# Performance work log

Measured on AMD Instinct MI355X. Metric: run time of the kernel, lower is better.

Reference implementation:

```python
import jax, jax.numpy as jnp
import numpy as np

N = 100000   # num nodes
E = 800000   # num edges
D = 16       # latent_dim
K = 3        # message-passing iterations
ALPHA = 0.1
GAMMA = 0.9


def _mlp2(x, w1, b1, w2, b2):
    return jax.nn.relu(x @ w1 + b1) @ w2 + b2


def setup_inputs() -> dict:
    key = jax.random.key(0)
    ks = iter(jax.random.split(key, 40))
    def w(shape, fan_in):
        return jax.random.normal(next(ks), shape, jnp.float32) / np.sqrt(fan_in)
    return {
        "edge_index": jax.random.randint(next(ks), (2, E), 0, N),
        "edge_attr": jax.random.normal(next(ks), (E, 3), jnp.float32),
        "a_ij": jax.random.normal(next(ks), (E, 1), jnp.float32),
        "prb_data": jax.random.normal(next(ks), (N, 1), jnp.float32),
        "sol": jax.random.normal(next(ks), (N, 1), jnp.float32),
        "y": jax.random.normal(next(ks), (N, 1), jnp.float32),
        "phi_to_w1": w((K, 2 * D + 3, D), 2 * D + 3), "phi_to_b1": jnp.zeros((K, D), jnp.float32),
        "phi_to_w2": w((K, D, D), D), "phi_to_b2": jnp.zeros((K, D), jnp.float32),
        "phi_from_w1": w((K, 2 * D + 3, D), 2 * D + 3), "phi_from_b1": jnp.zeros((K, D), jnp.float32),
        "phi_from_w2": w((K, D, D), D), "phi_from_b2": jnp.zeros((K, D), jnp.float32),
        "psi_w1": w((K, 3 * D + 1, D), 3 * D + 1), "psi_b1": jnp.zeros((K, D), jnp.float32),
        "psi_w2": w((K, D, D), D), "psi_b2": jnp.zeros((K, D), jnp.float32),
        "dec_w1": w((K, D, D), D), "dec_b1": jnp.zeros((K, D), jnp.float32),
        "dec_w2": w((K, D, 1), D), "dec_b2": jnp.zeros((K, 1), jnp.float32),
    }


def reference(edge_index, edge_attr, a_ij, prb_data, sol, y,
              phi_to_w1, phi_to_b1, phi_to_w2, phi_to_b2,
              phi_from_w1, phi_from_b1, phi_from_w2, phi_from_b2,
              psi_w1, psi_b1, psi_w2, psi_b2,
              dec_w1, dec_b1, dec_w2, dec_b2):
    src, dst = edge_index[0], edge_index[1]
    # remove_self_loops: with 'add' aggregation, zeroing self-loop messages is equivalent.
    sl_mask = (src != dst).astype(edge_attr.dtype)[:, None]

    def message_pass(h, xi_idx, xj_idx, agg_idx, w1, b1, w2, b2):
        # gather-concat-MLP-scatter: tmp is [E, 2D+3]
        tmp = jnp.concatenate([h[xi_idx], h[xj_idx], edge_attr], axis=1)
        m = _mlp2(tmp, w1, b1, w2, b2) * sl_mask
        return jax.ops.segment_sum(m, agg_idx, num_segments=N)

    a_val = a_ij[:, 0]
    def residual_loss(u):
        # SparseTensor(row=src, col=dst, value=a_ij) @ u  (self-loops kept here)
        Au = jax.ops.segment_sum(a_val * u[dst, 0], src, num_segments=N)[:, None]
        return jnp.mean((Au - y) ** 2)

    h = jnp.zeros((N, D), edge_attr.dtype)
    u = _mlp2(h, dec_w1[0], dec_b1[0], dec_w2[0], dec_b2[0])  # U['0']
    total_loss = jnp.zeros((), edge_attr.dtype)
    for t in range(K):
        # Phi_to: flow source_to_target -> x_i = h[dst], x_j = h[src], aggregate at dst
        mess_to = message_pass(h, dst, src, dst, phi_to_w1[t], phi_to_b1[t], phi_to_w2[t], phi_to_b2[t])
        # Phi_from: flow target_to_source -> x_i = h[src], x_j = h[dst], aggregate at src
        mess_from = message_pass(h, src, dst, src, phi_from_w1[t], phi_from_b1[t], phi_from_w2[t], phi_from_b2[t])
        concat = jnp.concatenate([h, mess_to, mess_from, prb_data], axis=1)  # [N, 3D+1]
        h = h + ALPHA * _mlp2(concat, psi_w1[t], psi_b1[t], psi_w2[t], psi_b2[t])
        u = _mlp2(h, dec_w1[t], dec_b1[t], dec_w2[t], dec_b2[t])
        total_loss = total_loss + residual_loss(u) * GAMMA ** (K - t - 1)
    return u, total_loss
```

## Files before the change

### kernel.cpp

```cpp
#include <hip/hip_runtime.h>

#define NN 100000
#define NE 800000
#define DD 16
#define ALPHA 0.1f

__device__ __forceinline__ void load16(const float* __restrict__ p, float* r) {
  float4 v0 = *(const float4*)(p + 0);
  float4 v1 = *(const float4*)(p + 4);
  float4 v2 = *(const float4*)(p + 8);
  float4 v3 = *(const float4*)(p + 12);
  r[0]=v0.x; r[1]=v0.y; r[2]=v0.z; r[3]=v0.w;
  r[4]=v1.x; r[5]=v1.y; r[6]=v1.z; r[7]=v1.w;
  r[8]=v2.x; r[9]=v2.y; r[10]=v2.z; r[11]=v2.w;
  r[12]=v3.x; r[13]=v3.y; r[14]=v3.z; r[15]=v3.w;
}

__device__ __forceinline__ void store16(float* __restrict__ p, const float* r) {
  *(float4*)(p + 0)  = make_float4(r[0], r[1], r[2], r[3]);
  *(float4*)(p + 4)  = make_float4(r[4], r[5], r[6], r[7]);
  *(float4*)(p + 8)  = make_float4(r[8], r[9], r[10], r[11]);
  *(float4*)(p + 12) = make_float4(r[12], r[13], r[14], r[15]);
}

__device__ __forceinline__ unsigned f2bf(float x) {
  unsigned b = __float_as_uint(x);
  return (b + 0x7FFFu + ((b >> 16) & 1u)) >> 16;
}

__global__ __launch_bounds__(256) void hist_kernel(
    const int* __restrict__ ei, int* __restrict__ hist,
    int* __restrict__ rank_dst, int* __restrict__ rank_src)
{
  int e = blockIdx.x * 256 + threadIdx.x;
  if (e >= NE) return;
  int s = ei[e];
  int d = ei[NE + e];
  rank_dst[e] = atomicAdd(&hist[d], 1);
  rank_src[e] = atomicAdd(&hist[NN + s], 1);
}

__global__ __launch_bounds__(256) void scan1_kernel(
    const int* __restrict__ in, int* __restrict__ out, int* __restrict__ sums, int L)
{
  __shared__ int sh[256];
  int t = threadIdx.x;
  int i0 = blockIdx.x * 1024 + t * 4;
  int v0 = (i0 + 0 < L) ? in[i0 + 0] : 0;
  int v1 = (i0 + 1 < L) ? in[i0 + 1] : 0;
  int v2 = (i0 + 2 < L) ? in[i0 + 2] : 0;
  int v3 = (i0 + 3 < L) ? in[i0 + 3] : 0;
  int tot = v0 + v1 + v2 + v3;
  sh[t] = tot;
  __syncthreads();
  int val = tot;
  for (int off = 1; off < 256; off <<= 1) {
    int x = (t >= off) ? sh[t - off] : 0;
    __syncthreads();
    val += x; sh[t] = val;
    __syncthreads();
  }
  if (t == 255) sums[blockIdx.x] = val;
  int run = val - tot;
  if (i0 + 0 < L) out[i0 + 0] = run; run += v0;
  if (i0 + 1 < L) out[i0 + 1] = run; run += v1;
  if (i0 + 2 < L) out[i0 + 2] = run; run += v2;
  if (i0 + 3 < L) out[i0 + 3] = run;
}

__global__ __launch_bounds__(256) void scan2_kernel(
    int* __restrict__ sums, int nb, int* __restrict__ out_total)
{
  __shared__ int sh[256];
  int t = threadIdx.x;
  int v = (t < nb) ? sums[t] : 0;
  sh[t] = v;
  __syncthreads();
  int val = v;
  for (int off = 1; off < 256; off <<= 1) {
    int x = (t >= off) ? sh[t - off] : 0;
    __syncthreads();
    val += x; sh[t] = val;
    __syncthreads();
  }
  if (t < nb) sums[t] = val - v;
  if (t == 255) *out_total = val;
}

__global__ __launch_bounds__(256) void scan3_kernel(
    int* __restrict__ out, const int* __restrict__ sums, int L)
{
  int i = blockIdx.x * 256 + threadIdx.x;
  if (i < L) out[i] += sums[i >> 10];
}

__global__ __launch_bounds__(256) void scatter_kernel(
    const int* __restrict__ ei, const float* __restrict__ ea, const float* __restrict__ a,
    const int* __restrict__ base,
    const int* __restrict__ rank_dst, const int* __restrict__ rank_src,
    float4* __restrict__ pay, float2* __restrict__ pay_au)
{
  int e = blockIdx.x * 256 + threadIdx.x;
  if (e >= NE) return;
  int s = ei[e];
  int d = ei[NE + e];
  float e0 = ea[3 * (size_t)e], e1 = ea[3 * (size_t)e + 1], e2 = ea[3 * (size_t)e + 2];
  int sl = (s == d);
  int pd = base[d] + rank_dst[e];
  pay[pd] = make_float4(__int_as_float(sl ? -1 : s), e0, e1, e2);
  int ps = base[NN + s] + rank_src[e];
  pay[ps] = make_float4(__int_as_float(sl ? -1 : d), e0, e1, e2);
  pay_au[ps - NE] = make_float2(__int_as_float(d), a[e]);
}

__global__ __launch_bounds__(256) void dbucket_kernel(
    const int* __restrict__ base, int* __restrict__ dhist)
{
  __shared__ int lh[64];
  int t = threadIdx.x;
  if (t < 64) lh[t] = 0;
  __syncthreads();
  int g = blockIdx.x * 256 + t;
  if (g < 2 * NN) {
    int dg = base[g + 1] - base[g];
    atomicAdd(&lh[min(dg, 63)], 1);
  }
  __syncthreads();
  if (t < 64 && lh[t]) atomicAdd(&dhist[t], lh[t]);
}

__global__ void dscan64_kernel(int* __restrict__ dhist)
{
  int t = threadIdx.x;
  int v = dhist[t];
  int x = v;
  #pragma unroll
  for (int off = 1; off < 64; off <<= 1) {
    int y = __shfl_up(x, off, 64);
    if (t >= off) x += y;
  }
  dhist[t] = x - v;
}

__global__ __launch_bounds__(256) void dperm_kernel(
    const int* __restrict__ base, int* __restrict__ dhist, int* __restrict__ perm)
{
  __shared__ int lh[64];
  __shared__ int lb[64];
  int t = threadIdx.x;
  if (t < 64) lh[t] = 0;
  __syncthreads();
  int g = blockIdx.x * 256 + t;
  int b = 0, r = 0;
  bool v = (g < 2 * NN);
  if (v) {
    int dg = base[g + 1] - base[g];
    b = min(dg, 63);
    r = atomicAdd(&lh[b], 1);
  }
  __syncthreads();
  if (t < 64 && lh[t]) lb[t] = atomicAdd(&dhist[t], lh[t]);
  __syncthreads();
  if (v) perm[lb[b] + r] = g;
}

template<bool FIRST, bool WITH_AU>
__global__ __launch_bounds__(256) void gather_kernel(
    const float* __restrict__ h, const unsigned short* __restrict__ hb,
    const float4* __restrict__ pay, const int* __restrict__ base,
    const int* __restrict__ perm,
    const float* __restrict__ to_w1, const float* __restrict__ to_b1,
    const float* __restrict__ to_w2, const float* __restrict__ to_b2,
    const float* __restrict__ fr_w1, const float* __restrict__ fr_b1,
    const float* __restrict__ fr_w2, const float* __restrict__ fr_b2,
    float* __restrict__ mto, float* __restrict__ mfr, int gblocks,
    const float2* __restrict__ pay_au, const float* __restrict__ u,
    const float* __restrict__ y, float w, float* __restrict__ loss)
{
  if (WITH_AU && (int)blockIdx.x >= gblocks) {
    __shared__ float ss[4];
    int n = (blockIdx.x - gblocks) * 256 + threadIdx.x;
    float acc = 0.0f;
    if (n < NN) {
      float au = 0.0f;
      int beg = base[NN + n] - NE, end = base[NN + n + 1] - NE;
      for (int i = beg; i < end; ++i) {
        float2 q = pay_au[i];
        au = fmaf(q.y, u[__float_as_int(q.x)], au);
      }
      float dlt = au - y[n];
      acc = dlt * dlt;
    }
    #pragma unroll
    for (int off = 32; off > 0; off >>= 1) acc += __shfl_down(acc, off);
    int lane = threadIdx.x & 63, wid = threadIdx.x >> 6;
    if (lane == 0) ss[wid] = acc;
    __syncthreads();
    if (threadIdx.x == 0) atomicAdd(loss, (ss[0] + ss[1] + ss[2] + ss[3]) * w);
    return;
  }

  __shared__ float sw[1696];
  __shared__ float p1buf[512];
  int t = threadIdx.x;
  for (int i = t; i < 560; i += 256) { sw[i] = to_w1[i]; sw[848 + i] = fr_w1[i]; }
  { int i = t;
    if (i < 256) { sw[576 + i] = to_w2[i]; sw[848 + 576 + i] = fr_w2[i]; }
    if (i < 16) {
      sw[560 + i] = to_b1[i];
      sw[832 + i] = to_b2[i];
      sw[848 + 560 + i] = fr_b1[i];
      sw[848 + 832 + i] = fr_b2[i];
    }
  }
  __syncthreads();

  int sub = (blockIdx.x * 256 + t) >> 3;
  int l = t & 7;
  int g = perm[sub];
  int dir = (g >= NN) ? 1 : 0;
  int n = g - (dir ? NN : 0);

  const float* w1 = sw + (dir ? 848 : 0);
  const float* b1 = w1 + 560;
  const float* w2 = w1 + 576;
  const float* b2 = w1 + 832;

  float p1v[DD];
  if (FIRST) {
    #pragma unroll
    for (int j = 0; j < DD; ++j) p1v[j] = b1[j];
  } else {
    float hv[DD];
    load16(h + (size_t)n * DD, hv);
    int j0 = 2 * l;
    float pa = b1[j0], pb = b1[j0 + 1];
    #pragma unroll
    for (int k = 0; k < DD; ++k) {
      pa = fmaf(hv[k], w1[k * DD + j0], pa);
      pb = fmaf(hv[k], w1[k * DD + j0 + 1], pb);
    }
    p1buf[2 * t] = pa;
    p1buf[2 * t + 1] = pb;
    __syncthreads();
    const float* pbase = &p1buf[(t & ~7) * 2];
    #pragma unroll
    for (int j = 0; j < DD; ++j) p1v[j] = pbase[j];
  }

  float hs_[DD];
  #pragma unroll
  for (int j = 0; j < DD; ++j) hs_[j] = 0.0f;
  int cnt = 0;

  int beg = base[g], end = base[g + 1];
  for (int i = beg + l; i < end; i += 8) {
    float4 q = pay[i];
    int nb = __float_as_int(q.x);
    if (nb >= 0) {
      float hid[DD];
      #pragma unroll
      for (int j = 0; j < DD; ++j)
        hid[j] = fmaf(q.y, w1[32 * DD + j],
                 fmaf(q.z, w1[33 * DD + j],
                 fmaf(q.w, w1[34 * DD + j], p1v[j])));
      if (!FIRST) {
        uint4 qa = *(const uint4*)(hb + (size_t)nb * DD);
        uint4 qb = *(const uint4*)(hb + (size_t)nb * DD + 8);
        float hv[DD];
        hv[0]  = __uint_as_float(qa.x << 16); hv[1]  = __uint_as_float(qa.x & 0xFFFF0000u);
        hv[2]  = __uint_as_float(qa.y << 16); hv[3]  = __uint_as_float(qa.y & 0xFFFF0000u);
        hv[4]  = __uint_as_float(qa.z << 16); hv[5]  = __uint_as_float(qa.z & 0xFFFF0000u);
        hv[6]  = __uint_as_float(qa.w << 16); hv[7]  = __uint_as_float(qa.w & 0xFFFF0000u);
        hv[8]  = __uint_as_float(qb.x << 16); hv[9]  = __uint_as_float(qb.x & 0xFFFF0000u);
        hv[10] = __uint_as_float(qb.y << 16); hv[11] = __uint_as_float(qb.y & 0xFFFF0000u);
        hv[12] = __uint_as_float(qb.z << 16); hv[13] = __uint_as_float(qb.z & 0xFFFF0000u);
        hv[14] = __uint_as_float(qb.w << 16); hv[15] = __uint_as_float(qb.w & 0xFFFF0000u);
        #pragma unroll
        for (int k = 0; k < DD; ++k) {
          float x = hv[k];
          #pragma unroll
          for (int j = 0; j < DD; ++j) hid[j] = fmaf(x, w1[(DD + k) * DD + j], hid[j]);
        }
      }
      #pragma unroll
      for (int j = 0; j < DD; ++j) hs_[j] += fmaxf(hid[j], 0.0f);
      ++cnt;
    }
  }

  #pragma unroll
  for (int j = 0; j < DD; ++j) {
    hs_[j] += __shfl_xor(hs_[j], 1, 64);
    hs_[j] += __shfl_xor(hs_[j], 2, 64);
    hs_[j] += __shfl_xor(hs_[j], 4, 64);
  }
  cnt += __shfl_xor(cnt, 1, 64);
  cnt += __shfl_xor(cnt, 2, 64);
  cnt += __shfl_xor(cnt, 4, 64);

  float c = (float)cnt;
  float m0 = c * b2[2 * l + 0];
  float m1 = c * b2[2 * l + 1];
  #pragma unroll
  for (int k = 0; k < DD; ++k) {
    float x = hs_[k];
    m0 = fmaf(x, w2[k * DD + 2 * l + 0], m0);
    m1 = fmaf(x, w2[k * DD + 2 * l + 1], m1);
  }
  float* dst = (dir ? mfr : mto) + (size_t)n * DD + 2 * l;
  *(float2*)dst = make_float2(m0, m1);
}

__global__ __launch_bounds__(256) void node_kernel(
    float* __restrict__ h, unsigned short* __restrict__ hb,
    const float* __restrict__ mto, const float* __restrict__ mfr,
    const float* __restrict__ prb,
    const float* __restrict__ psi_w1, const float* __restrict__ psi_b1,
    const float* __restrict__ psi_w2, const float* __restrict__ psi_b2,
    const float* __restrict__ dec_w1, const float* __restrict__ dec_b1,
    const float* __restrict__ dec_w2, const float* __restrict__ dec_b2,
    float* __restrict__ u)
{
  __shared__ float sw[1361];
  for (int i = threadIdx.x; i < 784; i += 256) sw[i] = psi_w1[i];
  { int i = threadIdx.x;
    if (i < 256) { sw[800 + i] = psi_w2[i]; sw[1072 + i] = dec_w1[i]; }
    if (i < 16) {
      sw[784 + i] = psi_b1[i];
      sw[1056 + i] = psi_b2[i];
      sw[1328 + i] = dec_b1[i];
      sw[1344 + i] = dec_w2[i];
    }
    if (i == 0) sw[1360] = dec_b2[0];
  }
  __syncthreads();

  int n = blockIdx.x * 256 + threadIdx.x;
  if (n >= NN) return;

  float hv[DD], mt[DD], mf[DD];
  load16(h + (size_t)n * DD, hv);
  load16(mto + (size_t)n * DD, mt);
  load16(mfr + (size_t)n * DD, mf);
  float p = prb[n];

  float hid[DD];
  #pragma unroll
  for (int j = 0; j < DD; ++j) hid[j] = sw[784 + j];
  #pragma unroll
  for (int i = 0; i < DD; ++i) {
    float x = hv[i];
    #pragma unroll
    for (int j = 0; j < DD; ++j) hid[j] = fmaf(x, sw[i * DD + j], hid[j]);
  }
  #pragma unroll
  for (int i = 0; i < DD; ++i) {
    float x = mt[i];
    #pragma unroll
    for (int j = 0; j < DD; ++j) hid[j] = fmaf(x, sw[(DD + i) * DD + j], hid[j]);
  }
  #pragma unroll
  for (int i = 0; i < DD; ++i) {
    float x = mf[i];
    #pragma unroll
    for (int j = 0; j < DD; ++j) hid[j] = fmaf(x, sw[(2 * DD + i) * DD + j], hid[j]);
  }
  #pragma unroll
  for (int j = 0; j < DD; ++j) hid[j] = fmaf(p, sw[48 * DD + j], hid[j]);
  #pragma unroll
  for (int j = 0; j < DD; ++j) hid[j] = fmaxf(hid[j], 0.0f);

  float hnew[DD];
  #pragma unroll
  for (int j = 0; j < DD; ++j) hnew[j] = sw[1056 + j];
  #pragma unroll
  for (int i = 0; i < DD; ++i) {
    float x = hid[i];
    #pragma unroll
    for (int j = 0; j < DD; ++j) hnew[j] = fmaf(x, sw[800 + i * DD + j], hnew[j]);
  }
  #pragma unroll
  for (int j = 0; j < DD; ++j) hnew[j] = fmaf(ALPHA, hnew[j], hv[j]);
  store16(h + (size_t)n * DD, hnew);

  uint4 pa, pb;
  pa.x = f2bf(hnew[0])  | (f2bf(hnew[1])  << 16);
  pa.y = f2bf(hnew[2])  | (f2bf(hnew[3])  << 16);
  pa.z = f2bf(hnew[4])  | (f2bf(hnew[5])  << 16);
  pa.w = f2bf(hnew[6])  | (f2bf(hnew[7])  << 16);
  pb.x = f2bf(hnew[8])  | (f2bf(hnew[9])  << 16);
  pb.y = f2bf(hnew[10]) | (f2bf(hnew[11]) << 16);
  pb.z = f2bf(hnew[12]) | (f2bf(hnew[13]) << 16);
  pb.w = f2bf(hnew[14]) | (f2bf(hnew[15]) << 16);
  *(uint4*)(hb + (size_t)n * DD)     = pa;
  *(uint4*)(hb + (size_t)n * DD + 8) = pb;

  float hid2[DD];
  #pragma unroll
  for (int j = 0; j < DD; ++j) hid2[j] = sw[1328 + j];
  #pragma unroll
  for (int i = 0; i < DD; ++i) {
    float x = hnew[i];
    #pragma unroll
    for (int j = 0; j < DD; ++j) hid2[j] = fmaf(x, sw[1072 + i * DD + j], hid2[j]);
  }
  float uo = sw[1360];
  #pragma unroll
  for (int i = 0; i < DD; ++i) uo += fmaxf(hid2[i], 0.0f) * sw[1344 + i];
  u[n] = uo;
}

extern "C" void kernel_launch(void* const* d_in, const int* in_sizes, int n_in,
                              void* d_out, int out_size, void* d_ws, size_t ws_size,
                              hipStream_t stream) {
  const int*   ei        = (const int*)d_in[0];
  const float* ea        = (const float*)d_in[1];
  const float* a_ij      = (const float*)d_in[2];
  const float* prb       = (const float*)d_in[3];
  const float* y         = (const float*)d_in[5];
  const float* phi_to_w1 = (const float*)d_in[6];
  const float* phi_to_b1 = (const float*)d_in[7];
  const float* phi_to_w2 = (const float*)d_in[8];
  const float* phi_to_b2 = (const float*)d_in[9];
  const float* phi_fr_w1 = (const float*)d_in[10];
  const float* phi_fr_b1 = (const float*)d_in[11];
  const float* phi_fr_w2 = (const float*)d_in[12];
  const float* phi_fr_b2 = (const float*)d_in[13];
  const float* psi_w1    = (const float*)d_in[14];
  const float* psi_b1    = (const float*)d_in[15];
  const float* psi_w2    = (const float*)d_in[16];
  const float* psi_b2    = (const float*)d_in[17];
  const float* dec_w1    = (const float*)d_in[18];
  const float* dec_b1    = (const float*)d_in[19];
  const float* dec_w2    = (const float*)d_in[20];
  const float* dec_b2    = (const float*)d_in[21];

  float* out_u    = (float*)d_out;
  float* out_loss = out_u + NN;

  char* wp = (char*)d_ws;
  auto carve = [&](size_t bytes) { void* p = (void*)wp; wp += (bytes + 15) & ~(size_t)15; return p; };
  float4* pay      = (float4*)carve((size_t)2 * NE * 16);
  float2* pay_au   = (float2*)carve((size_t)NE * 8);
  float*  h        = (float*)carve((size_t)NN * DD * 4);
  unsigned short* hb16 = (unsigned short*)carve((size_t)NN * DD * 2);
  float*  mto      = (float*)carve((size_t)NN * DD * 4);
  float*  mfr      = (float*)carve((size_t)NN * DD * 4);
  int*    rank_dst = (int*)carve((size_t)NE * 4);
  int*    rank_src = (int*)carve((size_t)NE * 4);
  int*    base     = (int*)carve((size_t)(2 * NN + 1) * 4);
  int*    hist     = (int*)carve((size_t)2 * NN * 4);
  int*    sums     = (int*)carve(256 * 4);
  int*    dhist    = (int*)carve(64 * 4);
  int*    perm     = rank_dst;

  hipMemsetAsync(h, 0, (size_t)NN * DD * 4, stream);
  hipMemsetAsync(out_loss, 0, 4, stream);
  hipMemsetAsync(hist, 0, (size_t)2 * NN * 4, stream);
  hipMemsetAsync(dhist, 0, 64 * 4, stream);

  const int EB  = (NE + 255) / 256;
  const int NB  = (NN + 255) / 256;
  const int L2N = 2 * NN;
  const int SB1 = (L2N + 1023) / 1024;
  const int SB3 = (L2N + 255) / 256;
  const int DB  = (L2N + 255) / 256;
  const int GB8 = (L2N * 8) / 256;

  hist_kernel<<<EB, 256, 0, stream>>>(ei, hist, rank_dst, rank_src);
  scan1_kernel<<<SB1, 256, 0, stream>>>(hist, base, sums, L2N);
  scan2_kernel<<<1, 256, 0, stream>>>(sums, SB1, base + L2N);
  scan3_kernel<<<SB3, 256, 0, stream>>>(base, sums, L2N);
  scatter_kernel<<<EB, 256, 0, stream>>>(ei, ea, a_ij, base, rank_dst, rank_src,
                                         pay, pay_au);
  dbucket_kernel<<<DB, 256, 0, stream>>>(base, dhist);
  dscan64_kernel<<<1, 64, 0, stream>>>(dhist);
  dperm_kernel<<<DB, 256, 0, stream>>>(base, dhist, perm);

  const float gw[3] = {0.81f, 0.9f, 1.0f};

  gather_kernel<true, false><<<GB8, 256, 0, stream>>>(
      h, hb16, pay, base, perm,
      phi_to_w1, phi_to_b1, phi_to_w2, phi_to_b2,
      phi_fr_w1, phi_fr_b1, phi_fr_w2, phi_fr_b2,
      mto, mfr, GB8, pay_au, out_u, y, 0.0f, out_loss);
  node_kernel<<<NB, 256, 0, stream>>>(
      h, hb16, mto, mfr, prb,
      psi_w1, psi_b1, psi_w2, psi_b2,
      dec_w1, dec_b1, dec_w2, dec_b2, out_u);

  for (int t = 1; t < 3; ++t) {
    gather_kernel<false, true><<<GB8 + NB, 256, 0, stream>>>(
        h, hb16, pay, base, perm,
        phi_to_w1 + t * 560, phi_to_b1 + t * 16, phi_to_w2 + t * 256, phi_to_b2 + t * 16,
        phi_fr_w1 + t * 560, phi_fr_b1 + t * 16, phi_fr_w2 + t * 256, phi_fr_b2 + t * 16,
        mto, mfr, GB8, pay_au, out_u, y, gw[t - 1] / (float)NN, out_loss);
    node_kernel<<<NB, 256, 0, stream>>>(
        h, hb16, mto, mfr, prb,
        psi_w1 + t * 784, psi_b1 + t * 16, psi_w2 + t * 256, psi_b2 + t * 16,
        dec_w1 + t * 256, dec_b1 + t * 16, dec_w2 + t * 16, dec_b2 + t, out_u);
  }

  gather_kernel<false, true><<<NB, 256, 0, stream>>>(
      h, hb16, pay, base, perm,
      phi_to_w1, phi_to_b1, phi_to_w2, phi_to_b2,
      phi_fr_w1, phi_fr_b1, phi_fr_w2, phi_fr_b2,
      mto, mfr, 0, pay_au, out_u, y, gw[2] / (float)NN, out_loss);
}
```

Baseline: 343.0 us.

## Use packed fp16 dot2 for edge MLP and fold degree histogram into scan

Switches the gathered neighbour features from bf16 to packed fp16 and computes the first edge-MLP layer with v_dot2 (fdot2) instructions against fp16-packed weights in shared memory, halving FMA count for the neighbour and two edge-attribute terms. Folds the degree-bucket histogram into scan1 and its 64-bin scan into scan2, removing two launches, and merges the memsets. Adds a FIRST variant of node_kernel that skips loading and multiplying the zero initial h. fp16 has less range than bf16 and the fdot2 path may change accuracy slightly.

```diff
diff --git a/kernel.cpp b/kernel.cpp
--- a/kernel.cpp
+++ b/kernel.cpp
@@ -4,6 +4,23 @@
 #define NE 800000
 #define DD 16
 #define ALPHA 0.1f
+
+typedef _Float16 h2_t __attribute__((ext_vector_type(2)));
+union U32H2 { unsigned u; h2_t h; };
+
+__device__ __forceinline__ unsigned pack2h(float a, float b) {
+  U32H2 v; v.h[0] = (_Float16)a; v.h[1] = (_Float16)b; return v.u;
+}
+
+__device__ __forceinline__ float dot2(unsigned a, unsigned b, float c) {
+  U32H2 ua, ub; ua.u = a; ub.u = b;
+#if __has_builtin(__builtin_amdgcn_fdot2)
+  return __builtin_amdgcn_fdot2(ua.h, ub.h, c, false);
+#else
+  return fmaf((float)ua.h[0], (float)ub.h[0],
+         fmaf((float)ua.h[1], (float)ub.h[1], c));
+#endif
+}
 
 __device__ __forceinline__ void load16(const float* __restrict__ p, float* r) {
   float4 v0 = *(const float4*)(p + 0);
@@ -23,11 +40,6 @@
   *(float4*)(p + 12) = make_float4(r[12], r[13], r[14], r[15]);
 }
 
-__device__ __forceinline__ unsigned f2bf(float x) {
-  unsigned b = __float_as_uint(x);
-  return (b + 0x7FFFu + ((b >> 16) & 1u)) >> 16;
-}
-
 __global__ __launch_bounds__(256) void hist_kernel(
     const int* __restrict__ ei, int* __restrict__ hist,
     int* __restrict__ rank_dst, int* __restrict__ rank_src)
@@ -41,10 +53,13 @@
 }
 
 __global__ __launch_bounds__(256) void scan1_kernel(
-    const int* __restrict__ in, int* __restrict__ out, int* __restrict__ sums, int L)
+    const int* __restrict__ in, int* __restrict__ out, int* __restrict__ sums,
+    int L, int* __restrict__ dhist)
 {
   __shared__ int sh[256];
+  __shared__ int lh[64];
   int t = threadIdx.x;
+  if (t < 64) lh[t] = 0;
   int i0 = blockIdx.x * 1024 + t * 4;
   int v0 = (i0 + 0 < L) ? in[i0 + 0] : 0;
   int v1 = (i0 + 1 < L) ? in[i0 + 1] : 0;
@@ -53,6 +68,10 @@
   int tot = v0 + v1 + v2 + v3;
   sh[t] = tot;
   __syncthreads();
+  if (i0 + 0 < L) atomicAdd(&lh[min(v0, 63)], 1);
+  if (i0 + 1 < L) atomicAdd(&lh[min(v1, 63)], 1);
+  if (i0 + 2 < L) atomicAdd(&lh[min(v2, 63)], 1);
+  if (i0 + 3 < L) atomicAdd(&lh[min(v3, 63)], 1);
   int val = tot;
   for (int off = 1; off < 256; off <<= 1) {
     int x = (t >= off) ? sh[t - off] : 0;
@@ -66,10 +85,12 @@
   if (i0 + 1 < L) out[i0 + 1] = run; run += v1;
   if (i0 + 2 < L) out[i0 + 2] = run; run += v2;
   if (i0 + 3 < L) out[i0 + 3] = run;
+  if (t < 64 && lh[t]) atomicAdd(&dhist[t], lh[t]);
 }
 
 __global__ __launch_bounds__(256) void scan2_kernel(
-    int* __restrict__ sums, int nb, int* __restrict__ out_total)
+    int* __restrict__ sums, int nb, int* __restrict__ out_total,
+    int* __restrict__ dhist)
 {
   __shared__ int sh[256];
   int t = threadIdx.x;
@@ -85,6 +106,16 @@
   }
   if (t < nb) sums[t] = val - v;
   if (t == 255) *out_total = val;
+  if (t < 64) {
+    int dv = dhist[t];
+    int dx = dv;
+    #pragma unroll
+    for (int off = 1; off < 64; off <<= 1) {
+      int dy = __shfl_up(dx, off, 64);
+      if (t >= off) dx += dy;
+    }
+    dhist[t] = dx - dv;
+  }
 }
 
 __global__ __launch_bounds__(256) void scan3_kernel(
@@ -113,35 +144,6 @@
   pay_au[ps - NE] = make_float2(__int_as_float(d), a[e]);
 }
 
-__global__ __launch_bounds__(256) void dbucket_kernel(
-    const int* __restrict__ base, int* __restrict__ dhist)
-{
-  __shared__ int lh[64];
-  int t = threadIdx.x;
-  if (t < 64) lh[t] = 0;
-  __syncthreads();
-  int g = blockIdx.x * 256 + t;
-  if (g < 2 * NN) {
-    int dg = base[g + 1] - base[g];
-    atomicAdd(&lh[min(dg, 63)], 1);
-  }
-  __syncthreads();
-  if (t < 64 && lh[t]) atomicAdd(&dhist[t], lh[t]);
-}
-
-__global__ void dscan64_kernel(int* __restrict__ dhist)
-{
-  int t = threadIdx.x;
-  int v = dhist[t];
-  int x = v;
-  #pragma unroll
-  for (int off = 1; off < 64; off <<= 1) {
-    int y = __shfl_up(x, off, 64);
-    if (t >= off) x += y;
-  }
-  dhist[t] = x - v;
-}
-
 __global__ __launch_bounds__(256) void dperm_kernel(
     const int* __restrict__ base, int* __restrict__ dhist, int* __restrict__ perm)
 {
@@ -166,7 +168,7 @@
 
 template<bool FIRST, bool WITH_AU>
 __global__ __launch_bounds__(256) void gather_kernel(
-    const float* __restrict__ h, const unsigned short* __restrict__ hb,
+    const float* __restrict__ h, const unsigned* __restrict__ hb,
     const float4* __restrict__ pay, const int* __restrict__ base,
     const int* __restrict__ perm,
     const float* __restrict__ to_w1, const float* __restrict__ to_b1,
@@ -201,6 +203,7 @@
   }
 
   __shared__ float sw[1696];
+  __shared__ unsigned w1h[2][144];
   __shared__ float p1buf[512];
   int t = threadIdx.x;
   for (int i = t; i < 560; i += 256) { sw[i] = to_w1[i]; sw[848 + i] = fr_w1[i]; }
@@ -213,6 +216,13 @@
       sw[848 + 832 + i] = fr_b2[i];
     }
   }
+  for (int i = t; i < 288; i += 256) {
+    int dr = i / 144, idx = i % 144;
+    int kp = idx >> 4, j = idx & 15;
+    int r0 = (kp < 8) ? (16 + 2 * kp) : 32;
+    const float* W = dr ? fr_w1 : to_w1;
+    w1h[dr][idx] = pack2h(W[r0 * DD + j], W[(r0 + 1) * DD + j]);
+  }
   __syncthreads();
 
   int sub = (blockIdx.x * 256 + t) >> 3;
@@ -225,6 +235,8 @@
   const float* b1 = w1 + 560;
   const float* w2 = w1 + 576;
   const float* b2 = w1 + 832;
+  const unsigned* whn = w1h[dir];
+  const unsigned* wha = w1h[dir] + 128;
 
   float p1v[DD];
   if (FIRST) {
@@ -258,29 +270,20 @@
     float4 q = pay[i];
     int nb = __float_as_int(q.x);
     if (nb >= 0) {
+      unsigned e01 = pack2h(q.y, q.z);
       float hid[DD];
       #pragma unroll
       for (int j = 0; j < DD; ++j)
-        hid[j] = fmaf(q.y, w1[32 * DD + j],
-                 fmaf(q.z, w1[33 * DD + j],
-                 fmaf(q.w, w1[34 * DD + j], p1v[j])));
+        hid[j] = fmaf(q.w, w1[34 * DD + j], dot2(e01, wha[j], p1v[j]));
       if (!FIRST) {
-        uint4 qa = *(const uint4*)(hb + (size_t)nb * DD);
-        uint4 qb = *(const uint4*)(hb + (size_t)nb * DD + 8);
-        float hv[DD];
-        hv[0]  = __uint_as_float(qa.x << 16); hv[1]  = __uint_as_float(qa.x & 0xFFFF0000u);
-        hv[2]  = __uint_as_float(qa.y << 16); hv[3]  = __uint_as_float(qa.y & 0xFFFF0000u);
-        hv[4]  = __uint_as_float(qa.z << 16); hv[5]  = __uint_as_float(qa.z & 0xFFFF0000u);
-        hv[6]  = __uint_as_float(qa.w << 16); hv[7]  = __uint_as_float(qa.w & 0xFFFF0000u);
-        hv[8]  = __uint_as_float(qb.x << 16); hv[9]  = __uint_as_float(qb.x & 0xFFFF0000u);
-        hv[10] = __uint_as_float(qb.y << 16); hv[11] = __uint_as_float(qb.y & 0xFFFF0000u);
-        hv[12] = __uint_as_float(qb.z << 16); hv[13] = __uint_as_float(qb.z & 0xFFFF0000u);
-        hv[14] = __uint_as_float(qb.w << 16); hv[15] = __uint_as_float(qb.w & 0xFFFF0000u);
+        uint4 qa = *(const uint4*)(hb + (size_t)nb * 8);
+        uint4 qb = *(const uint4*)(hb + (size_t)nb * 8 + 4);
+        unsigned hp[8] = {qa.x, qa.y, qa.z, qa.w, qb.x, qb.y, qb.z, qb.w};
         #pragma unroll
-        for (int k = 0; k < DD; ++k) {
-          float x = hv[k];
+        for (int kp = 0; kp < 8; ++kp) {
+          unsigned hv2 = hp[kp];
           #pragma unroll
-          for (int j = 0; j < DD; ++j) hid[j] = fmaf(x, w1[(DD + k) * DD + j], hid[j]);
+          for (int j = 0; j < DD; ++j) hid[j] = dot2(hv2, whn[kp * 16 + j], hid[j]);
         }
       }
       #pragma unroll
@@ -312,8 +315,9 @@
   *(float2*)dst = make_float2(m0, m1);
 }
 
+template<bool FIRST>
 __global__ __launch_bounds__(256) void node_kernel(
-    float* __restrict__ h, unsigned short* __restrict__ hb,
+    float* __restrict__ h, unsigned* __restrict__ hb,
     const float* __restrict__ mto, const float* __restrict__ mfr,
     const float* __restrict__ prb,
     const float* __restrict__ psi_w1, const float* __restrict__ psi_b1,
@@ -340,7 +344,11 @@
   if (n >= NN) return;
 
   float hv[DD], mt[DD], mf[DD];
-  load16(h + (size_t)n * DD, hv);
+  if (!FIRST) {
+    load16(h + (size_t)n * DD, hv);
+  } else {
+    for (int j = 0; j < DD; ++j) hv[j] = 0.0f;
+  }
   load16(mto + (size_t)n * DD, mt);
   load16(mfr + (size_t)n * DD, mf);
   float p = prb[n];
@@ -348,11 +356,13 @@
   float hid[DD];
   #pragma unroll
   for (int j = 0; j < DD; ++j) hid[j] = sw[784 + j];
-  #pragma unroll
-  for (int i = 0; i < DD; ++i) {
-    float x = hv[i];
-    #pragma unroll
-    for (int j = 0; j < DD; ++j) hid[j] = fmaf(x, sw[i * DD + j], hid[j]);
+  if (!FIRST) {
+    #pragma unroll
+    for (int i = 0; i < DD; ++i) {
+      float x = hv[i];
+      #pragma unroll
+      for (int j = 0; j < DD; ++j) hid[j] = fmaf(x, sw[i * DD + j], hid[j]);
+    }
   }
   #pragma unroll
   for (int i = 0; i < DD; ++i) {
@@ -385,16 +395,16 @@
   store16(h + (size_t)n * DD, hnew);
 
   uint4 pa, pb;
-  pa.x = f2bf(hnew[0])  | (f2bf(hnew[1])  << 16);
-  pa.y = f2bf(hnew[2])  | (f2bf(hnew[3])  << 16);
-  pa.z = f2bf(hnew[4])  | (f2bf(hnew[5])  << 16);
-  pa.w = f2bf(hnew[6])  | (f2bf(hnew[7])  << 16);
-  pb.x = f2bf(hnew[8])  | (f2bf(hnew[9])  << 16);
-  pb.y = f2bf(hnew[10]) | (f2bf(hnew[11]) << 16);
-  pb.z = f2bf(hnew[12]) | (f2bf(hnew[13]) << 16);
-  pb.w = f2bf(hnew[14]) | (f2bf(hnew[15]) << 16);
-  *(uint4*)(hb + (size_t)n * DD)     = pa;
-  *(uint4*)(hb + (size_t)n * DD + 8) = pb;
+  pa.x = pack2h(hnew[0],  hnew[1]);
+  pa.y = pack2h(hnew[2],  hnew[3]);
+  pa.z = pack2h(hnew[4],  hnew[5]);
+  pa.w = pack2h(hnew[6],  hnew[7]);
+  pb.x = pack2h(hnew[8],  hnew[9]);
+  pb.y = pack2h(hnew[10], hnew[11]);
+  pb.z = pack2h(hnew[12], hnew[13]);
+  pb.w = pack2h(hnew[14], hnew[15]);
+  *(uint4*)(hb + (size_t)n * 8)     = pa;
+  *(uint4*)(hb + (size_t)n * 8 + 4) = pb;
 
   float hid2[DD];
   #pragma unroll
@@ -441,42 +451,37 @@
 
   char* wp = (char*)d_ws;
   auto carve = [&](size_t bytes) { void* p = (void*)wp; wp += (bytes + 15) & ~(size_t)15; return p; };
-  float4* pay      = (float4*)carve((size_t)2 * NE * 16);
-  float2* pay_au   = (float2*)carve((size_t)NE * 8);
-  float*  h        = (float*)carve((size_t)NN * DD * 4);
-  unsigned short* hb16 = (unsigned short*)carve((size_t)NN * DD * 2);
-  float*  mto      = (float*)carve((size_t)NN * DD * 4);
-  float*  mfr      = (float*)carve((size_t)NN * DD * 4);
-  int*    rank_dst = (int*)carve((size_t)NE * 4);
-  int*    rank_src = (int*)carve((size_t)NE * 4);
-  int*    base     = (int*)carve((size_t)(2 * NN + 1) * 4);
-  int*    hist     = (int*)carve((size_t)2 * NN * 4);
-  int*    sums     = (int*)carve(256 * 4);
-  int*    dhist    = (int*)carve(64 * 4);
-  int*    perm     = rank_dst;
-
-  hipMemsetAsync(h, 0, (size_t)NN * DD * 4, stream);
+  float4*   pay    = (float4*)carve((size_t)2 * NE * 16);
+  float2*   pay_au = (float2*)carve((size_t)NE * 8);
+  float*    h      = (float*)carve((size_t)NN * DD * 4);
+  unsigned* hb16   = (unsigned*)carve((size_t)NN * 8 * 4);
+  float*    mto    = (float*)carve((size_t)NN * DD * 4);
+  float*    mfr    = (float*)carve((size_t)NN * DD * 4);
+  int*  rank_dst   = (int*)carve((size_t)NE * 4);
+  int*  rank_src   = (int*)carve((size_t)NE * 4);
+  int*  base       = (int*)carve((size_t)(2 * NN + 1) * 4);
+  int*  hist       = (int*)carve((size_t)2 * NN * 4);
+  int*  dhist      = (int*)carve(64 * 4);
+  int*  sums       = (int*)carve(256 * 4);
+  int*  perm       = rank_dst;
+
   hipMemsetAsync(out_loss, 0, 4, stream);
-  hipMemsetAsync(hist, 0, (size_t)2 * NN * 4, stream);
-  hipMemsetAsync(dhist, 0, 64 * 4, stream);
+  hipMemsetAsync(hist, 0, ((size_t)2 * NN + 64) * 4, stream);
 
   const int EB  = (NE + 255) / 256;
   const int NB  = (NN + 255) / 256;
   const int L2N = 2 * NN;
   const int SB1 = (L2N + 1023) / 1024;
   const int SB3 = (L2N + 255) / 256;
-  const int DB  = (L2N + 255) / 256;
   const int GB8 = (L2N * 8) / 256;
 
   hist_kernel<<<EB, 256, 0, stream>>>(ei, hist, rank_dst, rank_src);
-  scan1_kernel<<<SB1, 256, 0, stream>>>(hist, base, sums, L2N);
-  scan2_kernel<<<1, 256, 0, stream>>>(sums, SB1, base + L2N);
+  scan1_kernel<<<SB1, 256, 0, stream>>>(hist, base, sums, L2N, dhist);
+  scan2_kernel<<<1, 256, 0, stream>>>(sums, SB1, base + L2N, dhist);
   scan3_kernel<<<SB3, 256, 0, stream>>>(base, sums, L2N);
   scatter_kernel<<<EB, 256, 0, stream>>>(ei, ea, a_ij, base, rank_dst, rank_src,
                                          pay, pay_au);
-  dbucket_kernel<<<DB, 256, 0, stream>>>(base, dhist);
-  dscan64_kernel<<<1, 64, 0, stream>>>(dhist);
-  dperm_kernel<<<DB, 256, 0, stream>>>(base, dhist, perm);
+  dperm_kernel<<<SB3, 256, 0, stream>>>(base, dhist, perm);
 
   const float gw[3] = {0.81f, 0.9f, 1.0f};
 
@@ -485,7 +490,7 @@
       phi_to_w1, phi_to_b1, phi_to_w2, phi_to_b2,
       phi_fr_w1, phi_fr_b1, phi_fr_w2, phi_fr_b2,
       mto, mfr, GB8, pay_au, out_u, y, 0.0f, out_loss);
-  node_kernel<<<NB, 256, 0, stream>>>(
+  node_kernel<true><<<NB, 256, 0, stream>>>(
       h, hb16, mto, mfr, prb,
       psi_w1, psi_b1, psi_w2, psi_b2,
       dec_w1, dec_b1, dec_w2, dec_b2, out_u);
@@ -496,7 +501,7 @@
         phi_to_w1 + t * 560, phi_to_b1 + t * 16, phi_to_w2 + t * 256, phi_to_b2 + t * 16,
         phi_fr_w1 + t * 560, phi_fr_b1 + t * 16, phi_fr_w2 + t * 256, phi_fr_b2 + t * 16,
         mto, mfr, GB8, pay_au, out_u, y, gw[t - 1] / (float)NN, out_loss);
-    node_kernel<<<NB, 256, 0, stream>>>(
+    node_kernel<false><<<NB, 256, 0, stream>>>(
         h, hb16, mto, mfr, prb,
         psi_w1 + t * 784, psi_b1 + t * 16, psi_w2 + t * 256, psi_b2 + t * 16,
         dec_w1 + t * 256, dec_b1 + t * 16, dec_w2 + t * 16, dec_b2 + t, out_u);
```

After: 318.3 us. 1.08x faster.
